# Performance work log

Measured on AMD Instinct MI355X. Metric: run time of the kernel, lower is better.

Reference implementation:

```python
import jax, jax.numpy as jnp
import numpy as np

TEMPERATURE = 0.07


def setup_inputs() -> dict:
    key = jax.random.key(0)
    k1, k2 = jax.random.split(key)
    B, D = 8192, 256
    embeddings = jax.random.normal(k1, (B, D), dtype=jnp.float32)
    ids = jax.random.randint(k2, (B,), 0, 1024, dtype=jnp.int64 if jax.config.jax_enable_x64 else jnp.int32)
    return {"embeddings": embeddings, "ids": ids}


def reference(embeddings, ids):
    B = embeddings.shape[0]
    # L2-normalize rows (F.normalize with p=2, dim=1)
    emb = embeddings / jnp.maximum(jnp.linalg.norm(embeddings, axis=1, keepdims=True), 1e-12)
    sim = (emb @ emb.T) / TEMPERATURE                      # [B, B]
    eye = jnp.eye(B, dtype=bool)
    sim = jnp.where(eye, -jnp.inf, sim)
    exp_sim = jnp.exp(sim)                                  # diag -> 0
    pos_mask = (ids[:, None] == ids[None, :]) & ~eye        # [B, B]
    pos_sum = jnp.sum(jnp.where(pos_mask, exp_sim, 0.0), axis=1)  # [B]
    all_sum = jnp.sum(exp_sim, axis=1)                      # [B]
    valid = pos_mask.any(axis=1)
    per_row = -jnp.log(pos_sum / all_sum)
    loss = jnp.sum(jnp.where(valid, per_row, 0.0))
    n_valid = jnp.sum(valid.astype(jnp.float32))
    return loss / jnp.maximum(n_valid, 1.0)
```

## Files before the change

### kernel.cpp

```cpp
#include <hip/hip_runtime.h>
#include <hip/hip_bf16.h>
#include <hip/hip_fp8.h>

#define B_SZ 8192
#define D_SZ 256
#define NTILES 2080
#define GRID_SIM 1024
#define PRESCALE 4.539816004686735f

typedef __attribute__((ext_vector_type(4))) float f32x4;

__device__ __forceinline__ void async_copy16(const void* g, void* l) {
    __builtin_amdgcn_global_load_lds(
        (const __attribute__((address_space(1))) unsigned int*)g,
        (__attribute__((address_space(3))) unsigned int*)l,
        16, 0, 0);
}

__global__ __launch_bounds__(256) void norm_kernel(const float* __restrict__ emb,
                                                   unsigned char* __restrict__ nq,
                                                   float* __restrict__ sums) {
    sums[blockIdx.x * 64 + (threadIdx.x >> 2)] = 0.0f;

    const int wave = threadIdx.x >> 6, lane = threadIdx.x & 63;
    for (int g = blockIdx.x; g < B_SZ / 4; g += 256) {
        const int row = g * 4 + wave;
        const float4 v = ((const float4*)(emb + (size_t)row * D_SZ))[lane];
        float ss = v.x * v.x + v.y * v.y + v.z * v.z + v.w * v.w;
        #pragma unroll
        for (int m = 1; m < 64; m <<= 1) ss += __shfl_xor(ss, m, 64);
        float s = PRESCALE / fmaxf(sqrtf(ss), 1e-12f);
        __hip_fp8_e4m3 q0(v.x * s), q1(v.y * s), q2(v.z * s), q3(v.w * s);
        uchar4 o;
        o.x = q0.__x; o.y = q1.__x; o.z = q2.__x; o.w = q3.__x;
        ((uchar4*)(nq + (size_t)row * D_SZ))[lane] = o;
    }
}

__device__ __forceinline__ void decode_tile(int tb, int& i0, int& j0, bool& diag) {
    int bj = (int)((sqrtf(8.0f * tb + 1.0f) - 1.0f) * 0.5f);
    while ((bj + 1) * (bj + 2) / 2 <= tb) ++bj;
    while (bj * (bj + 1) / 2 > tb) --bj;
    const int bi = tb - bj * (bj + 1) / 2;
    i0 = bi * 128; j0 = bj * 128; diag = (bi == bj);
}

__device__ __forceinline__ void issue_stage_fp8(const unsigned char* __restrict__ N,
                                                int row0, int k0, unsigned char* sDst,
                                                int wave, int lane) {
    const int rowIn = lane >> 2;
    const int slot  = lane & 3;
    #pragma unroll
    for (int h = 0; h < 2; ++h) {
        const int rl  = wave * 32 + h * 16 + rowIn;
        const int c16 = slot ^ ((rl >> 1) & 3);
        async_copy16(N + (size_t)(row0 + rl) * D_SZ + k0 + c16 * 16,
                     sDst + (wave * 32 + h * 16) * 64);
    }
}

__global__ __launch_bounds__(256) void sim_kernel(const unsigned char* __restrict__ N,
                                                  const int* __restrict__ ids,
                                                  float* __restrict__ all_sum,
                                                  float* __restrict__ pos_sum) {
    __shared__ __align__(16) char smem[32768];
    unsigned char* sA = (unsigned char*)smem;
    unsigned char* sB = (unsigned char*)smem + 8192;
    float* rowAllPart = (float*)smem;
    float* rowPosPart = (float*)(smem + 16384);

    const int t    = threadIdx.x;
    const int wave = t >> 6, lane = t & 63;
    const int wy   = wave >> 1, wx = wave & 1;
    const int myc  = lane & 15;

    for (int tb = blockIdx.x; tb < NTILES; tb += GRID_SIM) {
        int i0, j0; bool diag;
        decode_tile(tb, i0, j0, diag);

        f32x4 acc[4][4];
        #pragma unroll
        for (int mi = 0; mi < 4; ++mi)
            #pragma unroll
            for (int ni = 0; ni < 4; ++ni)
                acc[mi][ni] = (f32x4){0.f, 0.f, 0.f, 0.f};

        for (int kk = 0; kk < 4; ++kk) {
            issue_stage_fp8(N, i0, kk * 64, sA, wave, lane);
            issue_stage_fp8(N, j0, kk * 64, sB, wave, lane);
            __syncthreads();

            #pragma unroll
            for (int ks = 0; ks < 2; ++ks) {
                const int C = ks * 4 + (lane >> 4);
                long long af[4], bf[4];
                #pragma unroll
                for (int mi = 0; mi < 4; ++mi) {
                    const int rr = wy * 64 + mi * 16 + (lane & 15);
                    const int s16 = (C >> 1) ^ ((rr >> 1) & 3);
                    af[mi] = *(const long long*)&sA[rr * 64 + s16 * 16 + (C & 1) * 8];
                }
                #pragma unroll
                for (int ni = 0; ni < 4; ++ni) {
                    const int rr = wx * 64 + ni * 16 + (lane & 15);
                    const int s16 = (C >> 1) ^ ((rr >> 1) & 3);
                    bf[ni] = *(const long long*)&sB[rr * 64 + s16 * 16 + (C & 1) * 8];
                }
                #pragma unroll
                for (int mi = 0; mi < 4; ++mi)
                    #pragma unroll
                    for (int ni = 0; ni < 4; ++ni)
                        acc[mi][ni] = __builtin_amdgcn_mfma_f32_16x16x32_fp8_fp8(
                            af[mi], bf[ni], acc[mi][ni], 0, 0, 0);
            }
            __syncthreads();
        }

        int idc[4];
        #pragma unroll
        for (int ni = 0; ni < 4; ++ni)
            idc[ni] = ids[j0 + wx * 64 + ni * 16 + myc];

        float cAll[4] = {0.f, 0.f, 0.f, 0.f};
        float cPos[4] = {0.f, 0.f, 0.f, 0.f};

        #pragma unroll
        for (int mi = 0; mi < 4; ++mi) {
            float rAll[4] = {0.f, 0.f, 0.f, 0.f};
            float rPos[4] = {0.f, 0.f, 0.f, 0.f};
            const int rbase = wy * 64 + mi * 16 + (lane >> 4) * 4;
            const int4 idr  = *(const int4*)&ids[i0 + rbase];
            #pragma unroll
            for (int ni = 0; ni < 4; ++ni) {
                const int cloc = wx * 64 + ni * 16 + myc;
                #pragma unroll
                for (int rg = 0; rg < 4; ++rg) {
                    const int lr = rbase + rg;
                    float e = __builtin_amdgcn_exp2f(acc[mi][ni][rg]);
                    if (diag && lr == cloc) e = 0.0f;
                    rAll[rg] += e; cAll[ni] += e;
                    const int idrv = (rg == 0) ? idr.x : (rg == 1) ? idr.y
                                   : (rg == 2) ? idr.z : idr.w;
                    if (idrv == idc[ni]) { rPos[rg] += e; cPos[ni] += e; }
                }
            }
            #pragma unroll
            for (int rg = 0; rg < 4; ++rg) {
                rowAllPart[(rbase + rg) * 32 + wx * 16 + myc] = rAll[rg];
                rowPosPart[(rbase + rg) * 32 + wx * 16 + myc] = rPos[rg];
            }
        }

        if (!diag) {
            #pragma unroll
            for (int ni = 0; ni < 4; ++ni) {
                cAll[ni] += __shfl_xor(cAll[ni], 16, 64);
                cAll[ni] += __shfl_xor(cAll[ni], 32, 64);
                cPos[ni] += __shfl_xor(cPos[ni], 16, 64);
                cPos[ni] += __shfl_xor(cPos[ni], 32, 64);
            }
            if (lane < 16) {
                #pragma unroll
                for (int ni = 0; ni < 4; ++ni) {
                    const int gc = j0 + wx * 64 + ni * 16 + lane;
                    atomicAdd(&all_sum[gc], cAll[ni]);
                    atomicAdd(&pos_sum[gc], cPos[ni]);
                }
            }
        }

        __syncthreads();
        {
            const int row = t & 127;
            const float* src = (t >= 128) ? rowPosPart : rowAllPart;
            float s = 0.0f;
            #pragma unroll
            for (int k8 = 0; k8 < 8; ++k8) {
                const int chunk = (k8 + (row & 7)) & 7;
                const float4 v = *(const float4*)&src[row * 32 + chunk * 4];
                s += v.x + v.y + v.z + v.w;
            }
            float* dst = (t >= 128) ? pos_sum : all_sum;
            atomicAdd(&dst[i0 + row], s);
        }
        __syncthreads();
    }
}

__global__ __launch_bounds__(256) void loss_kernel(const float* __restrict__ all_sum,
                                                   const float* __restrict__ pos_sum,
                                                   float* __restrict__ out) {
    float loss = 0.0f, cnt = 0.0f;
    for (int i = threadIdx.x; i < B_SZ; i += 256) {
        float p = pos_sum[i], a = all_sum[i];
        if (p > 0.0f) { loss += logf(a) - logf(p); cnt += 1.0f; }
    }
    #pragma unroll
    for (int m = 1; m < 64; m <<= 1) {
        loss += __shfl_xor(loss, m, 64);
        cnt  += __shfl_xor(cnt, m, 64);
    }
    __shared__ float sl[4], sc[4];
    int wave = threadIdx.x >> 6, lane = threadIdx.x & 63;
    if (lane == 0) { sl[wave] = loss; sc[wave] = cnt; }
    __syncthreads();
    if (threadIdx.x == 0) {
        float L = sl[0] + sl[1] + sl[2] + sl[3];
        float C = sc[0] + sc[1] + sc[2] + sc[3];
        out[0] = L / fmaxf(C, 1.0f);
    }
}

extern "C" void kernel_launch(void* const* d_in, const int* in_sizes, int n_in,
                              void* d_out, int out_size, void* d_ws, size_t ws_size,
                              hipStream_t stream) {
    const float* emb = (const float*)d_in[0];
    const int*   ids = (const int*)d_in[1];
    float*       out = (float*)d_out;

    float*         all_sum = (float*)d_ws;
    float*         pos_sum = all_sum + B_SZ;
    unsigned char* nq      = (unsigned char*)d_ws + 65536;

    norm_kernel<<<256, 256, 0, stream>>>(emb, nq, all_sum);
    sim_kernel<<<GRID_SIM, 256, 0, stream>>>(nq, ids, all_sum, pos_sum);
    loss_kernel<<<1, 256, 0, stream>>>(all_sum, pos_sum, out);
}
```

Before: 119.1 us.

## Give each wave private double-buffered LDS panels and drop block barriers

Each wave now loads its own 64-row A and B panels into a private LDS region. It double-buffers the K stages with async global-to-LDS copies and vmcnt waits instead of block-wide __syncthreads, and it prefetches the next tile's first stage during the last K stage. Row partial sums are reduced with shuffles and written with atomics directly, skipping the LDS row-reduction pass and zero pos atomics. The grid is halved to 512 blocks. The cost is duplicated global loads, since two waves share each A or B panel, plus 64KB of LDS per block and more row atomics. Relying on vmcnt alone without a barrier assumes each lane only reads LDS data written by its own wave's loads.

```diff
diff --git a/kernel.cpp b/kernel.cpp
--- a/kernel.cpp
+++ b/kernel.cpp
@@ -5,8 +5,11 @@
 #define B_SZ 8192
 #define D_SZ 256
 #define NTILES 2080
-#define GRID_SIM 1024
+#define GRID_SIM 512
 #define PRESCALE 4.539816004686735f
+
+#define WAIT_VM8 0x0F78
+#define WAIT_VM0 0x0F70
 
 typedef __attribute__((ext_vector_type(4))) float f32x4;
 
@@ -45,17 +48,44 @@
     i0 = bi * 128; j0 = bj * 128; diag = (bi == bj);
 }
 
-__device__ __forceinline__ void issue_stage_fp8(const unsigned char* __restrict__ N,
-                                                int row0, int k0, unsigned char* sDst,
-                                                int wave, int lane) {
+__device__ __forceinline__ void issue_panel(const unsigned char* __restrict__ src,
+                                            unsigned char* dst, int k0, int lane) {
     const int rowIn = lane >> 2;
     const int slot  = lane & 3;
     #pragma unroll
-    for (int h = 0; h < 2; ++h) {
-        const int rl  = wave * 32 + h * 16 + rowIn;
+    for (int q = 0; q < 4; ++q) {
+        const int rl  = q * 16 + rowIn;
         const int c16 = slot ^ ((rl >> 1) & 3);
-        async_copy16(N + (size_t)(row0 + rl) * D_SZ + k0 + c16 * 16,
-                     sDst + (wave * 32 + h * 16) * 64);
+        async_copy16(src + (size_t)rl * D_SZ + k0 + c16 * 16, dst + q * 1024);
+    }
+}
+
+__device__ __forceinline__ void compute_stage(const unsigned char* sAb,
+                                              const unsigned char* sBb,
+                                              f32x4 acc[4][4], int lane) {
+    #pragma unroll
+    for (int ks = 0; ks < 2; ++ks) {
+        const int C8 = ks * 4 + (lane >> 4);
+        const int hi = C8 >> 1, lo = (C8 & 1) * 8;
+        long long af[4], bf[4];
+        #pragma unroll
+        for (int mi = 0; mi < 4; ++mi) {
+            const int rl = mi * 16 + (lane & 15);
+            const int s16 = hi ^ ((rl >> 1) & 3);
+            af[mi] = *(const long long*)&sAb[rl * 64 + s16 * 16 + lo];
+        }
+        #pragma unroll
+        for (int ni = 0; ni < 4; ++ni) {
+            const int rl = ni * 16 + (lane & 15);
+            const int s16 = hi ^ ((rl >> 1) & 3);
+            bf[ni] = *(const long long*)&sBb[rl * 64 + s16 * 16 + lo];
+        }
+        #pragma unroll
+        for (int mi = 0; mi < 4; ++mi)
+            #pragma unroll
+            for (int ni = 0; ni < 4; ++ni)
+                acc[mi][ni] = __builtin_amdgcn_mfma_f32_16x16x32_fp8_fp8(
+                    af[mi], bf[ni], acc[mi][ni], 0, 0, 0);
     }
 }
 
@@ -63,20 +93,30 @@
                                                   const int* __restrict__ ids,
                                                   float* __restrict__ all_sum,
                                                   float* __restrict__ pos_sum) {
-    __shared__ __align__(16) char smem[32768];
-    unsigned char* sA = (unsigned char*)smem;
-    unsigned char* sB = (unsigned char*)smem + 8192;
-    float* rowAllPart = (float*)smem;
-    float* rowPosPart = (float*)(smem + 16384);
+    __shared__ __align__(16) unsigned char smem[65536];
 
     const int t    = threadIdx.x;
     const int wave = t >> 6, lane = t & 63;
     const int wy   = wave >> 1, wx = wave & 1;
     const int myc  = lane & 15;
-
-    for (int tb = blockIdx.x; tb < NTILES; tb += GRID_SIM) {
-        int i0, j0; bool diag;
-        decode_tile(tb, i0, j0, diag);
+    unsigned char* lds = smem + wave * 16384;
+
+    int tb = blockIdx.x;
+    int i0, j0; bool diag;
+    decode_tile(tb, i0, j0, diag);
+    const unsigned char* gA = N + (size_t)(i0 + wy * 64) * D_SZ;
+    const unsigned char* gB = N + (size_t)(j0 + wx * 64) * D_SZ;
+
+    issue_panel(gA, lds, 0, lane);
+    issue_panel(gB, lds + 4096, 0, lane);
+
+    while (true) {
+        const int ntb = tb + GRID_SIM;
+        const bool have_next = (ntb < NTILES);
+        int ni0 = i0, nj0 = j0; bool ndiag = diag;
+        if (have_next) decode_tile(ntb, ni0, nj0, ndiag);
+        const unsigned char* ngA = N + (size_t)(ni0 + wy * 64) * D_SZ;
+        const unsigned char* ngB = N + (size_t)(nj0 + wx * 64) * D_SZ;
 
         f32x4 acc[4][4];
         #pragma unroll
@@ -85,59 +125,46 @@
             for (int ni = 0; ni < 4; ++ni)
                 acc[mi][ni] = (f32x4){0.f, 0.f, 0.f, 0.f};
 
+        #pragma unroll
         for (int kk = 0; kk < 4; ++kk) {
-            issue_stage_fp8(N, i0, kk * 64, sA, wave, lane);
-            issue_stage_fp8(N, j0, kk * 64, sB, wave, lane);
-            __syncthreads();
-
-            #pragma unroll
-            for (int ks = 0; ks < 2; ++ks) {
-                const int C = ks * 4 + (lane >> 4);
-                long long af[4], bf[4];
-                #pragma unroll
-                for (int mi = 0; mi < 4; ++mi) {
-                    const int rr = wy * 64 + mi * 16 + (lane & 15);
-                    const int s16 = (C >> 1) ^ ((rr >> 1) & 3);
-                    af[mi] = *(const long long*)&sA[rr * 64 + s16 * 16 + (C & 1) * 8];
-                }
-                #pragma unroll
-                for (int ni = 0; ni < 4; ++ni) {
-                    const int rr = wx * 64 + ni * 16 + (lane & 15);
-                    const int s16 = (C >> 1) ^ ((rr >> 1) & 3);
-                    bf[ni] = *(const long long*)&sB[rr * 64 + s16 * 16 + (C & 1) * 8];
-                }
-                #pragma unroll
-                for (int mi = 0; mi < 4; ++mi)
-                    #pragma unroll
-                    for (int ni = 0; ni < 4; ++ni)
-                        acc[mi][ni] = __builtin_amdgcn_mfma_f32_16x16x32_fp8_fp8(
-                            af[mi], bf[ni], acc[mi][ni], 0, 0, 0);
-            }
-            __syncthreads();
-        }
-
+            unsigned char* cur = lds + (kk & 1) * 8192;
+            unsigned char* nxt = lds + ((kk + 1) & 1) * 8192;
+            if (kk < 3) {
+                issue_panel(gA, nxt, (kk + 1) * 64, lane);
+                issue_panel(gB, nxt + 4096, (kk + 1) * 64, lane);
+                __builtin_amdgcn_s_waitcnt(WAIT_VM8);
+            } else if (have_next) {
+                issue_panel(ngA, nxt, 0, lane);
+                issue_panel(ngB, nxt + 4096, 0, lane);
+                __builtin_amdgcn_s_waitcnt(WAIT_VM8);
+            } else {
+                __builtin_amdgcn_s_waitcnt(WAIT_VM0);
+            }
+            compute_stage(cur, cur + 4096, acc, lane);
+        }
+
+        const int R0 = i0 + wy * 64;
+        const int C0 = j0 + wx * 64;
         int idc[4];
         #pragma unroll
         for (int ni = 0; ni < 4; ++ni)
-            idc[ni] = ids[j0 + wx * 64 + ni * 16 + myc];
+            idc[ni] = ids[C0 + ni * 16 + myc];
 
         float cAll[4] = {0.f, 0.f, 0.f, 0.f};
         float cPos[4] = {0.f, 0.f, 0.f, 0.f};
 
         #pragma unroll
         for (int mi = 0; mi < 4; ++mi) {
+            const int rb = mi * 16 + (lane >> 4) * 4;
+            const int4 idr = *(const int4*)&ids[R0 + rb];
             float rAll[4] = {0.f, 0.f, 0.f, 0.f};
             float rPos[4] = {0.f, 0.f, 0.f, 0.f};
-            const int rbase = wy * 64 + mi * 16 + (lane >> 4) * 4;
-            const int4 idr  = *(const int4*)&ids[i0 + rbase];
             #pragma unroll
             for (int ni = 0; ni < 4; ++ni) {
-                const int cloc = wx * 64 + ni * 16 + myc;
                 #pragma unroll
                 for (int rg = 0; rg < 4; ++rg) {
-                    const int lr = rbase + rg;
                     float e = __builtin_amdgcn_exp2f(acc[mi][ni][rg]);
-                    if (diag && lr == cloc) e = 0.0f;
+                    if (diag && wy == wx && (rb + rg) == (ni * 16 + myc)) e = 0.0f;
                     rAll[rg] += e; cAll[ni] += e;
                     const int idrv = (rg == 0) ? idr.x : (rg == 1) ? idr.y
                                    : (rg == 2) ? idr.z : idr.w;
@@ -146,8 +173,18 @@
             }
             #pragma unroll
             for (int rg = 0; rg < 4; ++rg) {
-                rowAllPart[(rbase + rg) * 32 + wx * 16 + myc] = rAll[rg];
-                rowPosPart[(rbase + rg) * 32 + wx * 16 + myc] = rPos[rg];
+                #pragma unroll
+                for (int mm = 1; mm < 16; mm <<= 1) {
+                    rAll[rg] += __shfl_xor(rAll[rg], mm, 64);
+                    rPos[rg] += __shfl_xor(rPos[rg], mm, 64);
+                }
+            }
+            if (myc == 0) {
+                #pragma unroll
+                for (int rg = 0; rg < 4; ++rg) {
+                    atomicAdd(&all_sum[R0 + rb + rg], rAll[rg]);
+                    if (rPos[rg] != 0.0f) atomicAdd(&pos_sum[R0 + rb + rg], rPos[rg]);
+                }
             }
         }
 
@@ -162,28 +199,14 @@
             if (lane < 16) {
                 #pragma unroll
                 for (int ni = 0; ni < 4; ++ni) {
-                    const int gc = j0 + wx * 64 + ni * 16 + lane;
-                    atomicAdd(&all_sum[gc], cAll[ni]);
-                    atomicAdd(&pos_sum[gc], cPos[ni]);
-                }
-            }
-        }
-
-        __syncthreads();
-        {
-            const int row = t & 127;
-            const float* src = (t >= 128) ? rowPosPart : rowAllPart;
-            float s = 0.0f;
-            #pragma unroll
-            for (int k8 = 0; k8 < 8; ++k8) {
-                const int chunk = (k8 + (row & 7)) & 7;
-                const float4 v = *(const float4*)&src[row * 32 + chunk * 4];
-                s += v.x + v.y + v.z + v.w;
-            }
-            float* dst = (t >= 128) ? pos_sum : all_sum;
-            atomicAdd(&dst[i0 + row], s);
-        }
-        __syncthreads();
+                    atomicAdd(&all_sum[C0 + ni * 16 + lane], cAll[ni]);
+                    if (cPos[ni] != 0.0f) atomicAdd(&pos_sum[C0 + ni * 16 + lane], cPos[ni]);
+                }
+            }
+        }
+
+        if (!have_next) break;
+        tb = ntb; i0 = ni0; j0 = nj0; diag = ndiag; gA = ngA; gB = ngB;
     }
 }
 
```

After: 123.7 us. 1.04x slower.

## Software-pipeline fp8 tile loads through registers with double-buffered LDS

Applied to the files above, without the earlier changes.

Replaces the direct global-to-LDS async copies with register-staged loads. The next k-slice (or the first slice of the next tile) is prefetched into registers while the current slice is computed from one of two alternating LDS buffers. This removes one barrier per k-step, and global latency now overlaps MFMA work. It also skips pos_sum column atomics when the partial is zero. The cost is extra VGPR pressure and an explicit LDS store pass in place of the async path.

```diff
diff --git a/kernel.cpp b/kernel.cpp
--- a/kernel.cpp
+++ b/kernel.cpp
@@ -9,13 +9,6 @@
 #define PRESCALE 4.539816004686735f
 
 typedef __attribute__((ext_vector_type(4))) float f32x4;
-
-__device__ __forceinline__ void async_copy16(const void* g, void* l) {
-    __builtin_amdgcn_global_load_lds(
-        (const __attribute__((address_space(1))) unsigned int*)g,
-        (__attribute__((address_space(3))) unsigned int*)l,
-        16, 0, 0);
-}
 
 __global__ __launch_bounds__(256) void norm_kernel(const float* __restrict__ emb,
                                                    unsigned char* __restrict__ nq,
@@ -45,17 +38,29 @@
     i0 = bi * 128; j0 = bj * 128; diag = (bi == bj);
 }
 
-__device__ __forceinline__ void issue_stage_fp8(const unsigned char* __restrict__ N,
-                                                int row0, int k0, unsigned char* sDst,
-                                                int wave, int lane) {
-    const int rowIn = lane >> 2;
-    const int slot  = lane & 3;
+__device__ __forceinline__ void load_regs(int4 ra[2], int4 rb[2],
+                                          const unsigned char* __restrict__ N,
+                                          int i0, int j0, int k0,
+                                          int wave, int lane) {
+    const int rowIn = lane >> 2, slot = lane & 3;
     #pragma unroll
     for (int h = 0; h < 2; ++h) {
         const int rl  = wave * 32 + h * 16 + rowIn;
         const int c16 = slot ^ ((rl >> 1) & 3);
-        async_copy16(N + (size_t)(row0 + rl) * D_SZ + k0 + c16 * 16,
-                     sDst + (wave * 32 + h * 16) * 64);
+        ra[h] = *(const int4*)(N + (size_t)(i0 + rl) * D_SZ + k0 + c16 * 16);
+        rb[h] = *(const int4*)(N + (size_t)(j0 + rl) * D_SZ + k0 + c16 * 16);
+    }
+}
+
+__device__ __forceinline__ void store_stage(const int4 ra[2], const int4 rb[2],
+                                            unsigned char* bA, unsigned char* bB,
+                                            int wave, int lane) {
+    const int rowIn = lane >> 2, slot = lane & 3;
+    #pragma unroll
+    for (int h = 0; h < 2; ++h) {
+        const int rl = wave * 32 + h * 16 + rowIn;
+        *(int4*)&bA[rl * 64 + slot * 16] = ra[h];
+        *(int4*)&bB[rl * 64 + slot * 16] = rb[h];
     }
 }
 
@@ -63,20 +68,25 @@
                                                   const int* __restrict__ ids,
                                                   float* __restrict__ all_sum,
                                                   float* __restrict__ pos_sum) {
-    __shared__ __align__(16) char smem[32768];
-    unsigned char* sA = (unsigned char*)smem;
-    unsigned char* sB = (unsigned char*)smem + 8192;
-    float* rowAllPart = (float*)smem;
-    float* rowPosPart = (float*)(smem + 16384);
+    __shared__ __align__(16) unsigned char smem[32768];
 
     const int t    = threadIdx.x;
     const int wave = t >> 6, lane = t & 63;
     const int wy   = wave >> 1, wx = wave & 1;
     const int myc  = lane & 15;
 
-    for (int tb = blockIdx.x; tb < NTILES; tb += GRID_SIM) {
-        int i0, j0; bool diag;
-        decode_tile(tb, i0, j0, diag);
+    int tb = blockIdx.x;
+    int i0, j0; bool diag;
+    decode_tile(tb, i0, j0, diag);
+
+    int4 ra[2], rb[2];
+    load_regs(ra, rb, N, i0, j0, 0, wave, lane);
+
+    while (true) {
+        const int ntb = tb + GRID_SIM;
+        const bool have_next = (ntb < NTILES);
+        int ni0 = i0, nj0 = j0; bool ndiag = diag;
+        if (have_next) decode_tile(ntb, ni0, nj0, ndiag);
 
         f32x4 acc[4][4];
         #pragma unroll
@@ -85,26 +95,29 @@
             for (int ni = 0; ni < 4; ++ni)
                 acc[mi][ni] = (f32x4){0.f, 0.f, 0.f, 0.f};
 
+        #pragma unroll
         for (int kk = 0; kk < 4; ++kk) {
-            issue_stage_fp8(N, i0, kk * 64, sA, wave, lane);
-            issue_stage_fp8(N, j0, kk * 64, sB, wave, lane);
+            unsigned char* bA = smem + (kk & 1) * 16384;
+            unsigned char* bB = bA + 8192;
+            store_stage(ra, rb, bA, bB, wave, lane);
+            if (kk < 3)           load_regs(ra, rb, N, i0, j0, (kk + 1) * 64, wave, lane);
+            else if (have_next)   load_regs(ra, rb, N, ni0, nj0, 0, wave, lane);
             __syncthreads();
 
             #pragma unroll
             for (int ks = 0; ks < 2; ++ks) {
-                const int C = ks * 4 + (lane >> 4);
+                const int C8 = ks * 4 + (lane >> 4);
+                const int hi = C8 >> 1, lo = (C8 & 1) * 8;
                 long long af[4], bf[4];
                 #pragma unroll
                 for (int mi = 0; mi < 4; ++mi) {
                     const int rr = wy * 64 + mi * 16 + (lane & 15);
-                    const int s16 = (C >> 1) ^ ((rr >> 1) & 3);
-                    af[mi] = *(const long long*)&sA[rr * 64 + s16 * 16 + (C & 1) * 8];
+                    af[mi] = *(const long long*)&bA[rr * 64 + (hi ^ ((rr >> 1) & 3)) * 16 + lo];
                 }
                 #pragma unroll
                 for (int ni = 0; ni < 4; ++ni) {
                     const int rr = wx * 64 + ni * 16 + (lane & 15);
-                    const int s16 = (C >> 1) ^ ((rr >> 1) & 3);
-                    bf[ni] = *(const long long*)&sB[rr * 64 + s16 * 16 + (C & 1) * 8];
+                    bf[ni] = *(const long long*)&bB[rr * 64 + (hi ^ ((rr >> 1) & 3)) * 16 + lo];
                 }
                 #pragma unroll
                 for (int mi = 0; mi < 4; ++mi)
@@ -113,8 +126,11 @@
                         acc[mi][ni] = __builtin_amdgcn_mfma_f32_16x16x32_fp8_fp8(
                             af[mi], bf[ni], acc[mi][ni], 0, 0, 0);
             }
-            __syncthreads();
-        }
+        }
+        __syncthreads();
+
+        float* rowAllPart = (float*)smem;
+        float* rowPosPart = (float*)(smem + 16384);
 
         int idc[4];
         #pragma unroll
@@ -164,7 +180,7 @@
                 for (int ni = 0; ni < 4; ++ni) {
                     const int gc = j0 + wx * 64 + ni * 16 + lane;
                     atomicAdd(&all_sum[gc], cAll[ni]);
-                    atomicAdd(&pos_sum[gc], cPos[ni]);
+                    if (cPos[ni] != 0.0f) atomicAdd(&pos_sum[gc], cPos[ni]);
                 }
             }
         }
@@ -184,6 +200,9 @@
             atomicAdd(&dst[i0 + row], s);
         }
         __syncthreads();
+
+        if (!have_next) break;
+        tb = ntb; i0 = ni0; j0 = nj0; diag = ndiag;
     }
 }
 
```

After: 136.8 us. +14.9%, slower.
